# Performance work log

Measured on AMD Instinct MI355X. Metric: run time of the kernel, lower is better.

Reference implementation:

```python
import jax, jax.numpy as jnp
import numpy as np

EPS = 1e-5

def layernorm(x, g, b):
    mu = jnp.mean(x, axis=-1, keepdims=True)
    var = jnp.mean((x - mu) ** 2, axis=-1, keepdims=True)
    return (x - mu) * jax.lax.rsqrt(var + EPS) * g + b

def setup_inputs() -> dict:
    key = jax.random.key(0)
    B, T, C, H = 4, 2048, 1024, 16
    hs = C // H  # 64
    ks = jax.random.split(key, 16)
    s_in = 1.0 / np.sqrt(C)
    s_hid = 1.0 / np.sqrt(4 * C)
    return {
        "x":   jax.random.normal(ks[0], (B, T, C), jnp.float32),
        # per-head projections, stacked over heads: [H, C, hs]
        "Wq":  jax.random.normal(ks[1], (H, C, hs), jnp.float32) * s_in,
        "Wk":  jax.random.normal(ks[2], (H, C, hs), jnp.float32) * s_in,
        "Wv":  jax.random.normal(ks[3], (H, C, hs), jnp.float32) * s_in,
        # output projection [C, C] (concat of heads -> C)
        "Wo":  jax.random.normal(ks[4], (C, C), jnp.float32) * s_in,
        "bo":  jnp.zeros((C,), jnp.float32),
        # layernorm params
        "g1":  jnp.ones((C,), jnp.float32),
        "be1": jnp.zeros((C,), jnp.float32),
        "g2":  jnp.ones((C,), jnp.float32),
        "be2": jnp.zeros((C,), jnp.float32),
        # feed-forward: C -> 4C -> C
        "W1":  jax.random.normal(ks[5], (C, 4 * C), jnp.float32) * s_in,
        "b1":  jnp.zeros((4 * C,), jnp.float32),
        "W2":  jax.random.normal(ks[6], (4 * C, C), jnp.float32) * s_hid,
        "b2":  jnp.zeros((C,), jnp.float32),
    }

def reference(x, Wq, Wk, Wv, Wo, bo, g1, be1, g2, be2, W1, b1, W2, b2):
    B, T, C = x.shape
    H, _, hs = Wq.shape
    scale = hs ** -0.5

    # --- self-attention on ln1(x) ---
    xn = layernorm(x, g1, be1)
    q = jnp.einsum('btc,hcd->bhtd', xn, Wq)
    k = jnp.einsum('btc,hcd->bhtd', xn, Wk)
    v = jnp.einsum('btc,hcd->bhtd', xn, Wv)
    scores = jnp.einsum('bhtd,bhsd->bhts', q, k) * scale  # [B,H,T,T]
    causal = jnp.tril(jnp.ones((T, T), dtype=bool))
    scores = jnp.where(causal, scores, jnp.finfo(scores.dtype).min)
    wei = jax.nn.softmax(scores, axis=-1)
    out = jnp.einsum('bhts,bhsd->bhtd', wei, v)           # [B,H,T,hs]
    out = out.transpose(0, 2, 1, 3).reshape(B, T, H * hs)  # concat heads
    x = x + out @ Wo + bo

    # --- feed-forward on ln2(x) ---
    xn2 = layernorm(x, g2, be2)
    h = jax.nn.relu(xn2 @ W1 + b1)
    x = x + h @ W2 + b2
    return x
```

## Files before the change

kernel.cpp:

```cpp
#include <hip/hip_runtime.h>
#include <hip/hip_bf16.h>

typedef __hip_bfloat16 bf16;
typedef __attribute__((ext_vector_type(8))) short bf16x8;
typedef __attribute__((ext_vector_type(4))) short s16x4;
typedef __attribute__((ext_vector_type(4))) float f32x4;

__device__ __forceinline__ float b2f(bf16 v) { return __bfloat162float(v); }
__device__ __forceinline__ bf16  f2b(float v) { return __float2bfloat16(v); }
__device__ __forceinline__ float ldf(const bf16* p)  { return __bfloat162float(*p); }
__device__ __forceinline__ float ldf(const float* p) { return *p; }
__device__ __forceinline__ void  stf(bf16* p, float v)  { *p = __float2bfloat16(v); }
__device__ __forceinline__ void  stf(float* p, float v) { *p = v; }

__device__ __forceinline__ void load_lds16(const bf16* g, short* lds) {
    __builtin_amdgcn_global_load_lds(
        (const __attribute__((address_space(1))) unsigned int*)g,
        (__attribute__((address_space(3))) unsigned int*)lds, 16, 0, 0);
}

template<typename InT>
__global__ __launch_bounds__(256) void ln_kernel(const InT* __restrict__ x,
                                                 const float* __restrict__ g,
                                                 const float* __restrict__ b,
                                                 bf16* __restrict__ out)
{
    const int C = 1024;
    int row = blockIdx.x;
    int tid = threadIdx.x;
    const InT* xr = x + (size_t)row * C;

    float v[4];
    float s = 0.f, s2 = 0.f;
#pragma unroll
    for (int i = 0; i < 4; ++i) {
        float f = ldf(xr + tid + i * 256);
        v[i] = f; s += f; s2 += f * f;
    }
#pragma unroll
    for (int off = 32; off > 0; off >>= 1) {
        s  += __shfl_down(s,  off, 64);
        s2 += __shfl_down(s2, off, 64);
    }
    __shared__ float red[8];
    int wave = tid >> 6;
    if ((tid & 63) == 0) { red[wave] = s; red[wave + 4] = s2; }
    __syncthreads();
    float ts  = red[0] + red[1] + red[2] + red[3];
    float ts2 = red[4] + red[5] + red[6] + red[7];
    float mu  = ts * (1.f / 1024.f);
    float var = ts2 * (1.f / 1024.f) - mu * mu;
    float rstd = rsqrtf(var + 1e-5f);
#pragma unroll
    for (int i = 0; i < 4; ++i) {
        int c = tid + i * 256;
        out[(size_t)row * C + c] = f2b((v[i] - mu) * rstd * g[c] + b[c]);
    }
}

__global__ __launch_bounds__(256) void prep_weights(
    const float* __restrict__ Wq, const float* __restrict__ Wk,
    const float* __restrict__ Wv, const float* __restrict__ Wo,
    const float* __restrict__ W1, const float* __restrict__ W2,
    bf16* __restrict__ wqkvt, bf16* __restrict__ wot,
    bf16* __restrict__ w1t, bf16* __restrict__ w2t)
{
    __shared__ float t[32][33];
    int tx = threadIdx.x & 31, ty = threadIdx.x >> 5;
    int id = blockIdx.x;
    const float* in; bf16* out; int in_ld, out_ld, n0, k0;
    if (id < 3072) {
        const float* Ws[3] = {Wq, Wk, Wv};
        int m = id >> 10, r = id & 1023;
        int z = r >> 6, rt = r & 63;
        in = Ws[m] + z * 65536;
        out = wqkvt + (size_t)(m * 1024 + z * 64) * 1024;
        in_ld = 64; out_ld = 1024;
        n0 = (rt & 1) * 32; k0 = (rt >> 1) * 32;
    } else if (id < 4096) {
        int r = id - 3072;
        in = Wo; out = wot; in_ld = 1024; out_ld = 1024;
        n0 = (r & 31) * 32; k0 = (r >> 5) * 32;
    } else if (id < 8192) {
        int r = id - 4096;
        in = W1; out = w1t; in_ld = 4096; out_ld = 1024;
        n0 = (r & 127) * 32; k0 = (r >> 7) * 32;
    } else {
        int r = id - 8192;
        in = W2; out = w2t; in_ld = 1024; out_ld = 4096;
        n0 = (r & 31) * 32; k0 = (r >> 5) * 32;
    }
#pragma unroll
    for (int i = 0; i < 4; ++i)
        t[ty + i * 8][tx] = in[(size_t)(k0 + ty + i * 8) * in_ld + n0 + tx];
    __syncthreads();
#pragma unroll
    for (int i = 0; i < 4; ++i)
        out[(size_t)(n0 + ty + i * 8) * out_ld + k0 + tx] = f2b(t[tx][ty + i * 8]);
}

__global__ __launch_bounds__(256) void vt_kernel(
    const bf16* __restrict__ qkv, bf16* __restrict__ vt, int T)
{
    __shared__ float t[32][33];
    int tx = threadIdx.x & 31, ty = threadIdx.x >> 5;
    int z = blockIdx.z, b = z >> 4, h = z & 15;
    const bf16* in = qkv + (size_t)b * T * 3072 + 2048 + h * 64;
    bf16* out = vt + (size_t)z * 64 * T;
    int n0 = blockIdx.x * 32, k0 = blockIdx.y * 32;
#pragma unroll
    for (int i = 0; i < 4; ++i)
        t[ty + i * 8][tx] = b2f(in[(size_t)(k0 + ty + i * 8) * 3072 + n0 + tx]);
    __syncthreads();
#pragma unroll
    for (int i = 0; i < 4; ++i)
        out[(size_t)(n0 + ty + i * 8) * T + k0 + tx] = f2b(t[tx][ty + i * 8]);
}

template<bool RELU, bool HAS_BIAS, bool HAS_RES, typename ResT, typename OutT>
__global__ __launch_bounds__(256) void gemm_bt(
    const bf16* __restrict__ A, int lda,
    const bf16* __restrict__ Bt, int ldb,
    const float* __restrict__ bias,
    const ResT* __restrict__ res, int ldr,
    OutT* __restrict__ Cm, int ldc,
    int M, int N, int K)
{
    __shared__ short As[128 * 32];
    __shared__ short Bs[128 * 32];
    int tid = threadIdx.x, wv = tid >> 6, ln = tid & 63;

    int f = blockIdx.x + blockIdx.y * gridDim.x;
    int nby = gridDim.y;
    int by = f % nby, bx = f / nby;
    int bm0 = by * 128, bn0 = bx * 128;

    int wm = (wv & 1) * 64, wn = (wv >> 1) * 64;
    int quad = ln >> 4, lane15 = ln & 15;

    f32x4 acc[4][4] = {};

    int srow = ln >> 2;
    int scol = (((ln & 3) ^ (srow & 3)) * 8);
    int sw   = (quad ^ (lane15 & 3)) * 8;
    const bf16* Ab = A + (size_t)bm0 * lda;
    const bf16* Bb = Bt + (size_t)bn0 * ldb;

    for (int k0 = 0; k0 < K; k0 += 32) {
#pragma unroll
        for (int i = 0; i < 2; ++i) {
            int ch = wv + i * 4;
            load_lds16(Ab + (size_t)(ch * 16 + srow) * lda + k0 + scol, &As[ch * 16 * 32]);
            load_lds16(Bb + (size_t)(ch * 16 + srow) * ldb + k0 + scol, &Bs[ch * 16 * 32]);
        }
        __syncthreads();
        bf16x8 af[4], bfr[4];
#pragma unroll
        for (int mi = 0; mi < 4; ++mi)
            af[mi] = *(const bf16x8*)&As[(wm + mi * 16 + lane15) * 32 + sw];
#pragma unroll
        for (int ni = 0; ni < 4; ++ni)
            bfr[ni] = *(const bf16x8*)&Bs[(wn + ni * 16 + lane15) * 32 + sw];
#pragma unroll
        for (int mi = 0; mi < 4; ++mi)
#pragma unroll
            for (int ni = 0; ni < 4; ++ni)
                acc[mi][ni] = __builtin_amdgcn_mfma_f32_16x16x32_bf16(
                    af[mi], bfr[ni], acc[mi][ni], 0, 0, 0);
        __syncthreads();
    }

#pragma unroll
    for (int mi = 0; mi < 4; ++mi) {
#pragma unroll
        for (int r = 0; r < 4; ++r) {
            int gm = bm0 + wm + mi * 16 + quad * 4 + r;
#pragma unroll
            for (int ni = 0; ni < 4; ++ni) {
                int gn = bn0 + wn + ni * 16 + lane15;
                float v = acc[mi][ni][r];
                if (HAS_BIAS) v += bias[gn];
                if (HAS_RES)  v += ldf(res + (size_t)gm * ldr + gn);
                if (RELU)     v = fmaxf(v, 0.f);
                stf(Cm + (size_t)gm * ldc + gn, v);
            }
        }
    }
}

__global__ __launch_bounds__(512) void attn_kernel(
    const bf16* __restrict__ qkv, const bf16* __restrict__ vt,
    bf16* __restrict__ o, int T)
{
    const int LDQ = 3072;
    const int PS = 72;
    int qt = blockIdx.x, h = blockIdx.y, b = blockIdx.z;
    int tid = threadIdx.x, wv = tid >> 6, ln = tid & 63;
    int quad = ln >> 4, lane15 = ln & 15, r7 = lane15 & 7;

    __shared__ short KV[2][2][64 * 64];
    __shared__ short Ps[8][16 * PS];

    int lr = ln >> 3;
    int lc = ((ln & 7) ^ lr) * 8;

    const bf16* kbase = qkv + (size_t)(b * T) * LDQ + 1024 + h * 64;
    const bf16* vbase = vt + (size_t)((b * 16 + h) * 64) * T;

    short* Qarea = &KV[0][0][0];
#pragma unroll
    for (int i = 0; i < 2; ++i) {
        int ch = wv * 2 + i;
        load_lds16(qkv + (size_t)(b * T + qt * 128 + ch * 8 + lr) * LDQ + h * 64 + lc,
                   &Qarea[ch * 512]);
    }
    __syncthreads();
    bf16x8 qf[2];
#pragma unroll
    for (int ks = 0; ks < 2; ++ks)
        qf[ks] = *(const bf16x8*)&Qarea[(wv * 16 + lane15) * 64 + (((ks * 4 + quad) ^ r7) * 8)];
    __syncthreads();

    f32x4 oacc[4] = {};
    float mrun = -1e30f, lrun = 0.f;
    const float scale = 0.125f;
    int qmin = qt * 128 + wv * 16;
    int ntiles = 2 * qt + 2;

    load_lds16(kbase + (size_t)(0 * 64 + wv * 8 + lr) * LDQ + lc, &KV[0][0][wv * 8 * 64]);
    load_lds16(vbase + (size_t)(wv * 8 + lr) * T + 0 * 64 + lc, &KV[0][1][wv * 8 * 64]);

    for (int kt = 0; kt < ntiles; ++kt) {
        __syncthreads();
        if (kt + 1 < ntiles) {
            int nb = (kt + 1) & 1;
            load_lds16(kbase + (size_t)((kt + 1) * 64 + wv * 8 + lr) * LDQ + lc,
                       &KV[nb][0][wv * 8 * 64]);
            load_lds16(vbase + (size_t)(wv * 8 + lr) * T + (kt + 1) * 64 + lc,
                       &KV[nb][1][wv * 8 * 64]);
        }
        if (kt * 64 > qmin + 15) continue;

        const short* Ks = &KV[kt & 1][0][0];
        const short* Vs = &KV[kt & 1][1][0];

        f32x4 sacc[4] = {};
#pragma unroll
        for (int ks = 0; ks < 2; ++ks) {
            int so = ((ks * 4 + quad) ^ r7) * 8;
#pragma unroll
            for (int mi = 0; mi < 4; ++mi) {
                bf16x8 kf = *(const bf16x8*)&Ks[(mi * 16 + lane15) * 64 + so];
                sacc[mi] = __builtin_amdgcn_mfma_f32_16x16x32_bf16(kf, qf[ks], sacc[mi], 0, 0, 0);
            }
        }

        if (kt * 64 + 63 > qmin) {
            int ql = qmin + lane15;
#pragma unroll
            for (int mi = 0; mi < 4; ++mi)
#pragma unroll
                for (int r = 0; r < 4; ++r)
                    if (kt * 64 + mi * 16 + quad * 4 + r > ql) sacc[mi][r] = -3e38f;
        }

        float mx = sacc[0][0];
#pragma unroll
        for (int mi = 0; mi < 4; ++mi)
#pragma unroll
            for (int r = 0; r < 4; ++r) mx = fmaxf(mx, sacc[mi][r]);
        mx = fmaxf(mx, __shfl_xor(mx, 16, 64));
        mx = fmaxf(mx, __shfl_xor(mx, 32, 64));
        float mn = fmaxf(mrun, mx * scale);
        float alpha = __expf(mrun - mn);
        mrun = mn;

        float psum = 0.f;
#pragma unroll
        for (int mi = 0; mi < 4; ++mi) {
            float p[4];
#pragma unroll
            for (int r = 0; r < 4; ++r) {
                p[r] = __expf(fmaf(sacc[mi][r], scale, -mn));
                psum += p[r];
            }
            short tmp[4];
#pragma unroll
            for (int r = 0; r < 4; ++r) {
                bf16 pb = f2b(p[r]);
                tmp[r] = *(short*)&pb;
            }
            *(s16x4*)&Ps[wv][lane15 * PS + mi * 16 + quad * 4] = *(s16x4*)tmp;
        }
        lrun = lrun * alpha + psum;
#pragma unroll
        for (int di = 0; di < 4; ++di)
#pragma unroll
            for (int r = 0; r < 4; ++r) oacc[di][r] *= alpha;

#pragma unroll
        for (int ks = 0; ks < 2; ++ks) {
            int so = ((ks * 4 + quad) ^ r7) * 8;
            bf16x8 pf = *(const bf16x8*)&Ps[wv][lane15 * PS + ks * 32 + quad * 8];
#pragma unroll
            for (int di = 0; di < 4; ++di) {
                bf16x8 vf = *(const bf16x8*)&Vs[(di * 16 + lane15) * 64 + so];
                oacc[di] = __builtin_amdgcn_mfma_f32_16x16x32_bf16(vf, pf, oacc[di], 0, 0, 0);
            }
        }
    }

    lrun += __shfl_xor(lrun, 16, 64);
    lrun += __shfl_xor(lrun, 32, 64);
    float inv = 1.f / lrun;

    size_t row = (size_t)(b * T + qt * 128 + wv * 16 + lane15);
#pragma unroll
    for (int di = 0; di < 4; ++di) {
        short tmp[4];
#pragma unroll
        for (int r = 0; r < 4; ++r) {
            bf16 ob = f2b(oacc[di][r] * inv);
            tmp[r] = *(short*)&ob;
        }
        *(s16x4*)&o[row * 1024 + h * 64 + di * 16 + quad * 4] = *(s16x4*)tmp;
    }
}

extern "C" void kernel_launch(void* const* d_in, const int* in_sizes, int n_in,
                              void* d_out, int out_size, void* d_ws, size_t ws_size,
                              hipStream_t stream)
{
    (void)in_sizes; (void)n_in; (void)out_size; (void)ws_size;
    const float* x   = (const float*)d_in[0];
    const float* Wq  = (const float*)d_in[1];
    const float* Wk  = (const float*)d_in[2];
    const float* Wv  = (const float*)d_in[3];
    const float* Wo  = (const float*)d_in[4];
    const float* bo  = (const float*)d_in[5];
    const float* g1  = (const float*)d_in[6];
    const float* be1 = (const float*)d_in[7];
    const float* g2  = (const float*)d_in[8];
    const float* be2 = (const float*)d_in[9];
    const float* W1  = (const float*)d_in[10];
    const float* b1  = (const float*)d_in[11];
    const float* W2  = (const float*)d_in[12];
    const float* b2  = (const float*)d_in[13];

    const int T = 2048, M = 4 * T;
    const size_t MB = 1ull << 20;
    char* ws = (char*)d_ws;

    bf16*  xn    = (bf16*)(ws + 0 * MB);
    bf16*  qkv   = (bf16*)(ws + 16 * MB);
    bf16*  vt    = (bf16*)(ws + 64 * MB);
    bf16*  wqkvt = (bf16*)(ws + 80 * MB);
    bf16*  x1b   = (bf16*)(ws + 80 * MB);
    bf16*  wot   = (bf16*)(ws + 96 * MB);
    bf16*  xn2   = (bf16*)(ws + 96 * MB);
    bf16*  w1t   = (bf16*)(ws + 112 * MB);
    bf16*  w2t   = (bf16*)(ws + 120 * MB);
    bf16*  attnb = (bf16*)(ws + 0 * MB);
    bf16*  hb    = (bf16*)(ws + 0 * MB);

    dim3 blk(256);

    prep_weights<<<12288, blk, 0, stream>>>(Wq, Wk, Wv, Wo, W1, W2,
                                            wqkvt, wot, w1t, w2t);

    ln_kernel<float><<<M, blk, 0, stream>>>(x, g1, be1, xn);

    gemm_bt<false, false, false, float, bf16><<<dim3(24, 64), blk, 0, stream>>>(
        xn, 1024, wqkvt, 1024, nullptr, nullptr, 0, qkv, 3072, M, 3072, 1024);

    vt_kernel<<<dim3(2, T / 32, 64), blk, 0, stream>>>(qkv, vt, T);

    attn_kernel<<<dim3(T / 128, 16, 4), dim3(512), 0, stream>>>(qkv, vt, attnb, T);

    gemm_bt<false, true, true, float, bf16><<<dim3(8, 64), blk, 0, stream>>>(
        attnb, 1024, wot, 1024, bo, x, 1024, x1b, 1024, M, 1024, 1024);

    ln_kernel<bf16><<<M, blk, 0, stream>>>(x1b, g2, be2, xn2);

    gemm_bt<true, true, false, float, bf16><<<dim3(32, 64), blk, 0, stream>>>(
        xn2, 1024, w1t, 1024, b1, nullptr, 0, hb, 4096, M, 4096, 1024);

    gemm_bt<false, true, true, bf16, float><<<dim3(8, 64), blk, 0, stream>>>(
        hb, 4096, w2t, 4096, b2, x1b, 1024, (float*)d_out, 1024, M, 1024, 4096);
}
```

Before: 565.7 us.

## Double-buffer GEMM LDS tiles and add lazy rescale, reversed scheduling, priorities in attention

```diff
diff --git a/kernel.cpp b/kernel.cpp
--- a/kernel.cpp
+++ b/kernel.cpp
@@ -126,8 +126,8 @@
     OutT* __restrict__ Cm, int ldc,
     int M, int N, int K)
 {
-    __shared__ short As[128 * 32];
-    __shared__ short Bs[128 * 32];
+    __shared__ short As[2][128 * 32];
+    __shared__ short Bs[2][128 * 32];
     int tid = threadIdx.x, wv = tid >> 6, ln = tid & 63;
 
     int f = blockIdx.x + blockIdx.y * gridDim.x;
@@ -146,21 +146,34 @@
     const bf16* Ab = A + (size_t)bm0 * lda;
     const bf16* Bb = Bt + (size_t)bn0 * ldb;
 
+#pragma unroll
+    for (int i = 0; i < 2; ++i) {
+        int ch = wv + i * 4;
+        load_lds16(Ab + (size_t)(ch * 16 + srow) * lda + scol, &As[0][ch * 16 * 32]);
+        load_lds16(Bb + (size_t)(ch * 16 + srow) * ldb + scol, &Bs[0][ch * 16 * 32]);
+    }
+    __syncthreads();
+
+    int cur = 0;
     for (int k0 = 0; k0 < K; k0 += 32) {
-#pragma unroll
-        for (int i = 0; i < 2; ++i) {
-            int ch = wv + i * 4;
-            load_lds16(Ab + (size_t)(ch * 16 + srow) * lda + k0 + scol, &As[ch * 16 * 32]);
-            load_lds16(Bb + (size_t)(ch * 16 + srow) * ldb + k0 + scol, &Bs[ch * 16 * 32]);
-        }
-        __syncthreads();
+        if (k0 + 32 < K) {
+            int nb = cur ^ 1;
+#pragma unroll
+            for (int i = 0; i < 2; ++i) {
+                int ch = wv + i * 4;
+                load_lds16(Ab + (size_t)(ch * 16 + srow) * lda + k0 + 32 + scol,
+                           &As[nb][ch * 16 * 32]);
+                load_lds16(Bb + (size_t)(ch * 16 + srow) * ldb + k0 + 32 + scol,
+                           &Bs[nb][ch * 16 * 32]);
+            }
+        }
         bf16x8 af[4], bfr[4];
 #pragma unroll
         for (int mi = 0; mi < 4; ++mi)
-            af[mi] = *(const bf16x8*)&As[(wm + mi * 16 + lane15) * 32 + sw];
+            af[mi] = *(const bf16x8*)&As[cur][(wm + mi * 16 + lane15) * 32 + sw];
 #pragma unroll
         for (int ni = 0; ni < 4; ++ni)
-            bfr[ni] = *(const bf16x8*)&Bs[(wn + ni * 16 + lane15) * 32 + sw];
+            bfr[ni] = *(const bf16x8*)&Bs[cur][(wn + ni * 16 + lane15) * 32 + sw];
 #pragma unroll
         for (int mi = 0; mi < 4; ++mi)
 #pragma unroll
@@ -168,6 +181,7 @@
                 acc[mi][ni] = __builtin_amdgcn_mfma_f32_16x16x32_bf16(
                     af[mi], bfr[ni], acc[mi][ni], 0, 0, 0);
         __syncthreads();
+        cur ^= 1;
     }
 
 #pragma unroll
@@ -194,7 +208,8 @@
 {
     const int LDQ = 3072;
     const int PS = 72;
-    int qt = blockIdx.x, h = blockIdx.y, b = blockIdx.z;
+    int qt = (int)gridDim.x - 1 - (int)blockIdx.x;
+    int h = blockIdx.y, b = blockIdx.z;
     int tid = threadIdx.x, wv = tid >> 6, ln = tid & 63;
     int quad = ln >> 4, lane15 = ln & 15, r7 = lane15 & 7;
 
@@ -245,6 +260,7 @@
         const short* Vs = &KV[kt & 1][1][0];
 
         f32x4 sacc[4] = {};
+        __builtin_amdgcn_s_setprio(1);
 #pragma unroll
         for (int ks = 0; ks < 2; ++ks) {
             int so = ((ks * 4 + quad) ^ r7) * 8;
@@ -254,6 +270,7 @@
                 sacc[mi] = __builtin_amdgcn_mfma_f32_16x16x32_bf16(kf, qf[ks], sacc[mi], 0, 0, 0);
             }
         }
+        __builtin_amdgcn_s_setprio(0);
 
         if (kt * 64 + 63 > qmin) {
             int ql = qmin + lane15;
@@ -271,9 +288,18 @@
             for (int r = 0; r < 4; ++r) mx = fmaxf(mx, sacc[mi][r]);
         mx = fmaxf(mx, __shfl_xor(mx, 16, 64));
         mx = fmaxf(mx, __shfl_xor(mx, 32, 64));
-        float mn = fmaxf(mrun, mx * scale);
-        float alpha = __expf(mrun - mn);
-        mrun = mn;
+        float pmax = mx * scale;
+
+        if (!__all(pmax <= mrun + 8.f)) {
+            float mn = fmaxf(mrun, pmax);
+            float alpha = __expf(mrun - mn);
+            mrun = mn;
+            lrun *= alpha;
+#pragma unroll
+            for (int di = 0; di < 4; ++di)
+#pragma unroll
+                for (int r = 0; r < 4; ++r) oacc[di][r] *= alpha;
+        }
 
         float psum = 0.f;
 #pragma unroll
@@ -281,7 +307,7 @@
             float p[4];
 #pragma unroll
             for (int r = 0; r < 4; ++r) {
-                p[r] = __expf(fmaf(sacc[mi][r], scale, -mn));
+                p[r] = __expf(fmaf(sacc[mi][r], scale, -mrun));
                 psum += p[r];
             }
             short tmp[4];
@@ -292,12 +318,9 @@
             }
             *(s16x4*)&Ps[wv][lane15 * PS + mi * 16 + quad * 4] = *(s16x4*)tmp;
         }
-        lrun = lrun * alpha + psum;
-#pragma unroll
-        for (int di = 0; di < 4; ++di)
-#pragma unroll
-            for (int r = 0; r < 4; ++r) oacc[di][r] *= alpha;
-
+        lrun += psum;
+
+        __builtin_amdgcn_s_setprio(1);
 #pragma unroll
         for (int ks = 0; ks < 2; ++ks) {
             int so = ((ks * 4 + quad) ^ r7) * 8;
@@ -308,6 +331,7 @@
                 oacc[di] = __builtin_amdgcn_mfma_f32_16x16x32_bf16(vf, pf, oacc[di], 0, 0, 0);
             }
         }
+        __builtin_amdgcn_s_setprio(0);
     }
 
     lrun += __shfl_xor(lrun, 16, 64);
```

Measured after the change: 534.3 us. 1.06x faster.
